# Kernel tuning notes

Measured on AMD Instinct MI355X. Metric: run time of the kernel, lower is better.

The kernel has to match this reference:

```python
import jax, jax.numpy as jnp
import numpy as np
from jax import lax

IOU_THRESHOLD = 0.5
TOP = 1000


def setup_inputs() -> dict:
    key = jax.random.key(0)
    k1, k2, k3, k4, k5 = jax.random.split(key, 5)
    B, P = 16, 20000
    # valid (x1, y1, x2, y2) boxes on an ~800x800 image
    x1 = jax.random.uniform(k1, (B, P)) * 800.0
    y1 = jax.random.uniform(k2, (B, P)) * 800.0
    w = jax.random.uniform(k3, (B, P)) * 200.0 + 1.0
    h = jax.random.uniform(k4, (B, P)) * 200.0 + 1.0
    reg = jnp.stack([x1, y1, x1 + w, y1 + h], axis=-1)  # [B, P, 4]
    cls = jax.random.normal(k5, (B, P))                  # [B, P]
    return {"reg": reg, "cls": cls}


def _pairwise_iou(boxes):
    """boxes: [B, N, 4] (x1,y1,x2,y2) -> IoU [B, N, N]."""
    a = boxes[:, :, None, :]  # [B, N, 1, 4]
    b = boxes[:, None, :, :]  # [B, 1, N, 4]
    xx1 = jnp.maximum(a[..., 0], b[..., 0])
    yy1 = jnp.maximum(a[..., 1], b[..., 1])
    xx2 = jnp.minimum(a[..., 2], b[..., 2])
    yy2 = jnp.minimum(a[..., 3], b[..., 3])
    inter = jnp.clip(xx2 - xx1, 0.0) * jnp.clip(yy2 - yy1, 0.0)
    area_a = (a[..., 2] - a[..., 0]) * (a[..., 3] - a[..., 1])
    area_b = (b[..., 2] - b[..., 0]) * (b[..., 3] - b[..., 1])
    return inter / (area_a + area_b - inter)


def reference(reg, cls):
    B = cls.shape[0]
    # sort by confidence descending, gather boxes, keep top
    order = jnp.argsort(-cls, axis=1)                      # [B, P]
    sorted_cls = jnp.take_along_axis(cls, order, axis=1)[:, :TOP]            # [B, N]
    sorted_reg = jnp.take_along_axis(reg, order[:, :, None], axis=1)[:, :TOP]  # [B, N, 4]
    N = sorted_cls.shape[1]

    iou = _pairwise_iou(sorted_reg)                        # [B, N, N]

    # sequential greedy suppression: if box i still kept, drop boxes with IoU>=thr
    def body(mask, i):
        keep_i = mask[:, i]                                # [B]
        tmp = iou[:, i, :] < IOU_THRESHOLD                 # [B, N]
        upd = (mask & tmp).at[:, i].set(True)
        new_mask = jnp.where(keep_i[:, None], upd, mask)
        return new_mask, None

    mask0 = jnp.ones((B, N), dtype=bool)
    mask, _ = lax.scan(body, mask0, jnp.arange(N))

    out_reg = jnp.where(mask[:, :, None], sorted_reg, 0.0)
    out_cls = jnp.where(mask, sorted_cls, 0.0)
    return out_reg, out_cls
```

## Files before the change

### kernel.cpp

```cpp
#include <hip/hip_runtime.h>
#include <stdint.h>

#define BATCH 16
#define NPTS  20000
#define TOPK  1000
#define NKPT  20
#define NBIN  2048
#define NCOPY 4
#define CANDCAP 2048

__device__ __forceinline__ uint32_t key_desc(float f) {
    uint32_t u = __float_as_uint(f);
    uint32_t m = (u & 0x80000000u) ? ~u : (u | 0x80000000u);
    return ~m;
}

__device__ __forceinline__ float key_undo(uint32_t k) {
    uint32_t m = ~k;
    uint32_t u = (m & 0x80000000u) ? (m & 0x7FFFFFFFu) : ~m;
    return __uint_as_float(u);
}

__device__ __forceinline__ void push64(bool pred, uint64_t val, int* cntr,
                                       uint64_t* list, int lane) {
    uint64_t mask = __ballot(pred);
    if (mask) {
        int first = __ffsll((long long)mask) - 1;
        int base = 0;
        if (lane == first) base = atomicAdd(cntr, (int)__popcll(mask));
        base = __shfl(base, first);
        if (pred) {
            int off = (int)__popcll(mask & ((1ull << lane) - 1ull));
            list[base + off] = val;
        }
    }
}

__device__ __forceinline__ void wave_select(const uint64_t* lst, int n, int r,
                                            uint64_t* out, int wave, int lane) {
    if (wave == 0) {
        uint64_t my = (lane < n) ? lst[lane] : ~0ull;
        int rank = 0;
        for (int i = 0; i < n; ++i) { uint64_t o = __shfl(my, i); if (o < my) rank++; }
        if (lane < n && rank == r) *out = my;
    }
}

__device__ uint64_t bit_search(const uint32_t* kreg, uint64_t known, uint64_t kmask,
                               int startbit, uint32_t r, int* sh_c,
                               int tid, int lane) {
    for (int bit = startbit; bit >= 0; --bit) {
        if (tid == 0) *sh_c = 0;
        __syncthreads();
        uint32_t local = 0;
        #pragma unroll
        for (int j = 0; j < NKPT; ++j) {
            int p = tid + j * 1024;
            uint64_t k64 = ((uint64_t)kreg[j] << 32) | (uint32_t)p;
            if (p < NPTS && (k64 & kmask) == known && !((k64 >> bit) & 1ull)) local++;
        }
        #pragma unroll
        for (int d = 1; d < 64; d <<= 1) local += __shfl_xor(local, d);
        if (lane == 0 && local) atomicAdd(sh_c, (int)local);
        __syncthreads();
        uint32_t c0 = (uint32_t)*sh_c;
        if (r >= c0) { known |= 1ull << bit; r -= c0; }
        kmask |= 1ull << bit;
        __syncthreads();
    }
    return known;
}

__device__ __forceinline__ void hist_scan_find(
    uint32_t (*wh)[NBIN], uint32_t* wsum, uint32_t* wpre,
    int* sh_T, int* sh_r, int* sh_binc,
    int tid, int wave, int lane, uint32_t r)
{
    uint32_t m0 = 0, m1 = 0;
    #pragma unroll
    for (int cpy = 0; cpy < NCOPY; ++cpy) { m0 += wh[cpy][2*tid]; m1 += wh[cpy][2*tid+1]; }
    uint32_t s = m0 + m1, x = s;
    #pragma unroll
    for (int d = 1; d < 64; d <<= 1) { uint32_t t = __shfl_up(x, d); if (lane >= d) x += t; }
    if (lane == 63) wsum[wave] = x;
    __syncthreads();
    if (wave == 0 && lane < 16) {
        uint32_t v = wsum[lane], y = v;
        #pragma unroll
        for (int d = 1; d < 16; d <<= 1) { uint32_t t = __shfl_up(y, d); if (lane >= d) y += t; }
        wpre[lane] = y - v;
    }
    __syncthreads();
    uint32_t e = wpre[wave] + (x - s);
    if (r >= e && r < e + s) {
        if (r < e + m0) { *sh_T = 2*tid;     *sh_r = (int)(r - e);      *sh_binc = (int)m0; }
        else            { *sh_T = 2*tid + 1; *sh_r = (int)(r - e - m0); *sh_binc = (int)m1; }
    }
}

__global__ __launch_bounds__(1024, 4) void topk_kernel(
    const float* __restrict__ reg, const float* __restrict__ cls,
    float4* __restrict__ ws_boxes, float* __restrict__ ws_cls)
{
    __shared__ uint32_t whist[NCOPY][NBIN];
    __shared__ uint32_t wsum[16], wpre[16];
    __shared__ int      sh_T, sh_r, sh_binc, sh_cnt, sh_c;
    __shared__ uint64_t sh_kthkey;
    __shared__ uint64_t cand[CANDCAP];
    __shared__ uint64_t cand2[64];
    __shared__ uint64_t sel[1024];

    const int b = blockIdx.x, tid = threadIdx.x;
    const int wave = tid >> 6, lane = tid & 63;
    const float* c = cls + (size_t)b * NPTS;

    if (tid == 0) { sh_cnt = 0; }

    #pragma unroll
    for (int i = 0; i < NCOPY * NBIN / 1024; ++i) ((uint32_t*)whist)[tid + i * 1024] = 0;
    uint32_t kreg[NKPT];
    #pragma unroll
    for (int j = 0; j < NKPT; ++j) {
        int p = tid + j * 1024;
        kreg[j] = (p < NPTS) ? key_desc(c[p]) : 0xFFFFFFFFu;
    }
    __syncthreads();

    #pragma unroll
    for (int j = 0; j < NKPT; ++j) {
        int p = tid + j * 1024;
        if (p < NPTS) atomicAdd(&whist[wave >> 2][kreg[j] >> 21], 1u);
    }
    __syncthreads();
    hist_scan_find(whist, wsum, wpre, &sh_T, &sh_r, &sh_binc, tid, wave, lane, TOPK - 1);
    __syncthreads();
    const uint32_t T1 = (uint32_t)sh_T;
    int r = sh_r;
    const int cnt1 = sh_binc;
    uint64_t known = (uint64_t)T1 << 53;

    if (cnt1 <= 64) {
        __syncthreads();
        #pragma unroll
        for (int j = 0; j < NKPT; ++j) {
            int p = tid + j * 1024;
            push64(p < NPTS && (kreg[j] >> 21) == T1,
                   ((uint64_t)kreg[j] << 32) | (uint32_t)p, &sh_cnt, cand2, lane);
        }
        __syncthreads();
        wave_select(cand2, cnt1, r, &sh_kthkey, wave, lane);
        __syncthreads();
    } else if (cnt1 <= CANDCAP) {
        __syncthreads();
        #pragma unroll
        for (int j = 0; j < NKPT; ++j) {
            int p = tid + j * 1024;
            push64(p < NPTS && (kreg[j] >> 21) == T1,
                   ((uint64_t)kreg[j] << 32) | (uint32_t)p, &sh_cnt, cand, lane);
        }
        __syncthreads();
        #pragma unroll
        for (int i = 0; i < NCOPY * NBIN / 1024; ++i) ((uint32_t*)whist)[tid + i * 1024] = 0;
        __syncthreads();
        for (int i = tid; i < cnt1; i += 1024)
            atomicAdd(&whist[wave >> 2][(uint32_t)((cand[i] >> 42) & 2047)], 1u);
        __syncthreads();
        hist_scan_find(whist, wsum, wpre, &sh_T, &sh_r, &sh_binc, tid, wave, lane, (uint32_t)r);
        __syncthreads();
        const uint32_t T2 = (uint32_t)sh_T; r = sh_r;
        const int cnt2 = sh_binc;
        known |= (uint64_t)T2 << 42;
        if (cnt2 <= 64) {
            if (tid == 0) sh_cnt = 0;
            __syncthreads();
            for (int i = tid; i < cnt1; i += 1024)
                push64(((cand[i] >> 42) & 2047) == (uint64_t)T2,
                       cand[i], &sh_cnt, cand2, lane);
            __syncthreads();
            wave_select(cand2, cnt2, r, &sh_kthkey, wave, lane);
            __syncthreads();
        } else {
            uint64_t kk = bit_search(kreg, known, 0xFFFFFC0000000000ull, 41,
                                     (uint32_t)r, &sh_c, tid, lane);
            if (tid == 0) sh_kthkey = kk;
            __syncthreads();
        }
    } else {
        uint64_t kk = bit_search(kreg, known, 0xFFE0000000000000ull, 52,
                                 (uint32_t)r, &sh_c, tid, lane);
        if (tid == 0) sh_kthkey = kk;
        __syncthreads();
    }
    const uint64_t kthkey = sh_kthkey;

    if (tid == 0) sh_cnt = 0;
    sel[tid] = ~0ull;
    __syncthreads();
    #pragma unroll
    for (int j = 0; j < NKPT; ++j) {
        int p = tid + j * 1024;
        uint64_t key = ((uint64_t)kreg[j] << 32) | (uint32_t)p;
        push64(p < NPTS && key <= kthkey, key, &sh_cnt, sel, lane);
    }
    __syncthreads();

    uint64_t e = sel[tid];
    #pragma unroll
    for (int k = 2; k <= 64; k <<= 1) {
        #pragma unroll
        for (int j = k >> 1; j >= 1; j >>= 1) {
            uint64_t o = __shfl_xor(e, j);
            uint64_t lo = (e < o) ? e : o;
            uint64_t hi = (e < o) ? o : e;
            bool dir   = (lane & k) == 0;
            bool upper = (lane & j) != 0;
            e = (upper == dir) ? hi : lo;
        }
    }
    sel[tid] = e;
    __syncthreads();
    int grank = lane;
    #pragma unroll 1
    for (int w2 = 0; w2 < 16; ++w2) {
        if (w2 == wave) continue;
        const uint64_t* bp = &sel[w2 * 64];
        int cf = 0;
        #pragma unroll
        for (int s = 32; s >= 1; s >>= 1) {
            int t2 = cf + s;
            if (bp[t2 - 1] < e) cf = t2;
        }
        if (bp[cf] < e) cf++;
        grank += cf;
    }
    if (e != ~0ull) {
        int p = (int)(e & 0xFFFFFFFFull);
        ws_boxes[b * TOPK + grank] = ((const float4*)reg)[(size_t)b * NPTS + p];
        ws_cls[b * TOPK + grank] = key_undo((uint32_t)(e >> 32));
    }
}

__global__ __launch_bounds__(256) void iou_kernel(
    const float4* __restrict__ ws_boxes, uint32_t* __restrict__ suppT)
{
    __shared__ float4 boxes[TOPK];
    __shared__ float  areas[TOPK];
    const int b   = blockIdx.y;
    const int j   = blockIdx.x;
    const int tid = threadIdx.x;
    for (int i = tid; i < TOPK; i += 256) {
        float4 v = ws_boxes[b * TOPK + i];
        boxes[i] = v;
        areas[i] = (v.z - v.x) * (v.w - v.y);
    }
    __syncthreads();

    const int lane = tid & 63;
    const int wave = tid >> 6;
    uint32_t* t = suppT + (size_t)b * 32 * 1024;

    for (int k = wave; ; k += 4) {
        const int i = j + (k << 4);
        if (i >= TOPK) break;
        float4 a = boxes[i];
        float areaA = areas[i];
        uint64_t mine = 0;
        for (int w2 = i >> 6; w2 < 16; ++w2) {
            int col = (w2 << 6) | lane;
            bool sup = false;
            if (col < TOPK) {
                float4 bb = boxes[col];
                float xx1 = fmaxf(a.x, bb.x);
                float yy1 = fmaxf(a.y, bb.y);
                float xx2 = fminf(a.z, bb.z);
                float yy2 = fminf(a.w, bb.w);
                float iw = fmaxf(xx2 - xx1, 0.0f);
                float ih = fmaxf(yy2 - yy1, 0.0f);
                float inter = iw * ih;
                float iou = inter / (areaA + areas[col] - inter);
                sup = (iou >= 0.5f);
            }
            uint64_t m = __ballot(sup);
            if (lane == w2) mine = m;
        }
        if (lane < 16) {
            t[(2 * lane + 0) * 1024 + i] = (uint32_t)(mine & 0xFFFFFFFFull);
            t[(2 * lane + 1) * 1024 + i] = (uint32_t)(mine >> 32);
        }
    }
}

__global__ __launch_bounds__(64) void sweep_kernel(
    const uint32_t* __restrict__ suppT, const float4* __restrict__ ws_boxes,
    const float* __restrict__ ws_cls, float* __restrict__ out)
{
    const int b    = blockIdx.x;
    const int lane = threadIdx.x;
    const int myw  = lane & 31;
    const uint32_t* base = suppT + (size_t)b * 32 * 1024;

    uint32_t remv = 0, keptw = 0;
    uint4 dgA[8], clA[8], dgB[8], clB[8];

#define LOADG(W, DG, CL) { \
    const uint4* dp_ = (const uint4*)(base + (W) * 1024 + (W) * 32); \
    const uint4* cp_ = (const uint4*)(base + myw * 1024 + (W) * 32); \
    _Pragma("unroll") \
    for (int k_ = 0; k_ < 8; ++k_) { DG[k_] = dp_[k_]; CL[k_] = cp_[k_]; } }

#define STEP(D, C, BBIT) { \
    uint32_t live_ = (((~cur) >> (BBIT)) & 1u) & (uint32_t)((BBIT) < nb); \
    uint32_t msk_ = (uint32_t)0 - live_; \
    kmask |= (live_ << (BBIT)); \
    cur  |= (D) & msk_; \
    acc  |= (C) & msk_; }

#define PROC(W, DG, CL) { \
    const int nb = ((W) == 31) ? (TOPK - 31 * 32) : 32; \
    uint32_t cur = __shfl(remv, (W)); \
    uint32_t kmask = 0, acc = 0; \
    _Pragma("unroll") \
    for (int k_ = 0; k_ < 8; ++k_) { \
        STEP(DG[k_].x, CL[k_].x, 4 * k_ + 0); \
        STEP(DG[k_].y, CL[k_].y, 4 * k_ + 1); \
        STEP(DG[k_].z, CL[k_].z, 4 * k_ + 2); \
        STEP(DG[k_].w, CL[k_].w, 4 * k_ + 3); \
    } \
    remv |= acc; \
    if (myw == (W)) keptw = kmask; }

    LOADG(0, dgA, clA);
    #pragma unroll 1
    for (int w2 = 0; w2 < 16; ++w2) {
        const int wE = 2 * w2, wO = 2 * w2 + 1;
        LOADG(wO, dgB, clB);
        PROC(wE, dgA, clA);
        if (wO + 1 < 32) LOADG(wO + 1, dgA, clA);
        PROC(wO, dgB, clB);
    }

    __shared__ uint32_t skept[32];
    if (lane < 32) skept[lane] = keptw;
    __syncthreads();

    const float4* bx = ws_boxes + (size_t)b * TOPK;
    const float*  bc = ws_cls + (size_t)b * TOPK;
    float4* outr = (float4*)out + (size_t)b * TOPK;
    float*  outc = out + (size_t)BATCH * TOPK * 4 + (size_t)b * TOPK;
    for (int i = lane; i < TOPK; i += 64) {
        uint32_t keep = (skept[i >> 5] >> (i & 31)) & 1u;
        float4 v = bx[i];
        float cv = bc[i];
        outr[i] = keep ? v : make_float4(0.f, 0.f, 0.f, 0.f);
        outc[i] = keep ? cv : 0.0f;
    }
#undef LOADG
#undef STEP
#undef PROC
}

extern "C" void kernel_launch(void* const* d_in, const int* in_sizes, int n_in,
                              void* d_out, int out_size, void* d_ws, size_t ws_size,
                              hipStream_t stream) {
    (void)in_sizes; (void)n_in; (void)out_size; (void)ws_size;
    const float* reg = (const float*)d_in[0];
    const float* cls = (const float*)d_in[1];
    float* out = (float*)d_out;
    char* ws = (char*)d_ws;

    float4*   ws_boxes = (float4*)ws;
    float*    ws_cls   = (float*)(ws + 256000);
    uint32_t* suppT    = (uint32_t*)(ws + 320000);

    topk_kernel<<<dim3(BATCH), dim3(1024), 0, stream>>>(reg, cls, ws_boxes, ws_cls);
    iou_kernel<<<dim3(16, BATCH), dim3(256), 0, stream>>>(ws_boxes, suppT);
    sweep_kernel<<<dim3(BATCH), dim3(64), 0, stream>>>(suppT, ws_boxes, ws_cls, out);
}
```

Baseline: 83.35 us.

## Simplify top-k threshold selection with single-pass candidate split and brute-force rank

The top-k kernel now fuses key loading with the first histogram pass. It also replaces the second-level histogram refinement with one push pass. That pass sends keys from bins below the threshold bin straight into the selection buffer and collects threshold-bin keys into a candidate list. The exact k-th key is then found by an O(n^2) rank count over the candidates, which removes several barriers and the second histogram round but costs quadratic work when the threshold bin is large. The launch-bounds occupancy hint is also dropped.

```diff
diff --git a/kernel.cpp b/kernel.cpp
--- a/kernel.cpp
+++ b/kernel.cpp
@@ -36,16 +36,6 @@
     }
 }
 
-__device__ __forceinline__ void wave_select(const uint64_t* lst, int n, int r,
-                                            uint64_t* out, int wave, int lane) {
-    if (wave == 0) {
-        uint64_t my = (lane < n) ? lst[lane] : ~0ull;
-        int rank = 0;
-        for (int i = 0; i < n; ++i) { uint64_t o = __shfl(my, i); if (o < my) rank++; }
-        if (lane < n && rank == r) *out = my;
-    }
-}
-
 __device__ uint64_t bit_search(const uint32_t* kreg, uint64_t known, uint64_t kmask,
                                int startbit, uint32_t r, int* sh_c,
                                int tid, int lane) {
@@ -98,111 +88,78 @@
     }
 }
 
-__global__ __launch_bounds__(1024, 4) void topk_kernel(
+__global__ __launch_bounds__(1024) void topk_kernel(
     const float* __restrict__ reg, const float* __restrict__ cls,
     float4* __restrict__ ws_boxes, float* __restrict__ ws_cls)
 {
     __shared__ uint32_t whist[NCOPY][NBIN];
     __shared__ uint32_t wsum[16], wpre[16];
-    __shared__ int      sh_T, sh_r, sh_binc, sh_cnt, sh_c;
+    __shared__ int      sh_T, sh_r, sh_binc, sh_cnt, sh_cnt2, sh_c;
     __shared__ uint64_t sh_kthkey;
     __shared__ uint64_t cand[CANDCAP];
-    __shared__ uint64_t cand2[64];
     __shared__ uint64_t sel[1024];
 
     const int b = blockIdx.x, tid = threadIdx.x;
     const int wave = tid >> 6, lane = tid & 63;
     const float* c = cls + (size_t)b * NPTS;
 
-    if (tid == 0) { sh_cnt = 0; }
-
+    if (tid == 0) { sh_cnt = 0; sh_cnt2 = 0; }
+    sel[tid] = ~0ull;
     #pragma unroll
     for (int i = 0; i < NCOPY * NBIN / 1024; ++i) ((uint32_t*)whist)[tid + i * 1024] = 0;
+    __syncthreads();
+
     uint32_t kreg[NKPT];
     #pragma unroll
     for (int j = 0; j < NKPT; ++j) {
         int p = tid + j * 1024;
-        kreg[j] = (p < NPTS) ? key_desc(c[p]) : 0xFFFFFFFFu;
-    }
-    __syncthreads();
-
-    #pragma unroll
-    for (int j = 0; j < NKPT; ++j) {
-        int p = tid + j * 1024;
-        if (p < NPTS) atomicAdd(&whist[wave >> 2][kreg[j] >> 21], 1u);
+        uint32_t k = (p < NPTS) ? key_desc(c[p]) : 0xFFFFFFFFu;
+        kreg[j] = k;
+        if (p < NPTS) atomicAdd(&whist[wave >> 2][k >> 21], 1u);
     }
     __syncthreads();
     hist_scan_find(whist, wsum, wpre, &sh_T, &sh_r, &sh_binc, tid, wave, lane, TOPK - 1);
     __syncthreads();
     const uint32_t T1 = (uint32_t)sh_T;
-    int r = sh_r;
-    const int cnt1 = sh_binc;
-    uint64_t known = (uint64_t)T1 << 53;
-
-    if (cnt1 <= 64) {
-        __syncthreads();
+    const int r = sh_r, cnt1 = sh_binc;
+
+    if (cnt1 <= CANDCAP) {
         #pragma unroll
         for (int j = 0; j < NKPT; ++j) {
             int p = tid + j * 1024;
-            push64(p < NPTS && (kreg[j] >> 21) == T1,
-                   ((uint64_t)kreg[j] << 32) | (uint32_t)p, &sh_cnt, cand2, lane);
-        }
-        __syncthreads();
-        wave_select(cand2, cnt1, r, &sh_kthkey, wave, lane);
-        __syncthreads();
-    } else if (cnt1 <= CANDCAP) {
-        __syncthreads();
+            uint32_t k = kreg[j];
+            uint64_t key = ((uint64_t)k << 32) | (uint32_t)p;
+            bool valid = (p < NPTS);
+            uint32_t bin = k >> 21;
+            push64(valid && bin < T1, key, &sh_cnt, sel, lane);
+            push64(valid && bin == T1, key, &sh_cnt2, cand, lane);
+        }
+        __syncthreads();
+        for (int i = tid; i < cnt1; i += 1024) {
+            uint64_t e = cand[i];
+            int rk = 0;
+            for (int q = 0; q < cnt1; ++q) rk += (cand[q] < e) ? 1 : 0;
+            if (rk == r) sh_kthkey = e;
+        }
+        __syncthreads();
+        const uint64_t kth = sh_kthkey;
+        for (int i = tid; i < cnt1; i += 1024)
+            push64(cand[i] <= kth, cand[i], &sh_cnt, sel, lane);
+        __syncthreads();
+    } else {
+        uint64_t kk = bit_search(kreg, (uint64_t)T1 << 53, 0xFFE0000000000000ull,
+                                 52, (uint32_t)r, &sh_c, tid, lane);
+        if (tid == 0) { sh_kthkey = kk; sh_cnt = 0; }
+        __syncthreads();
+        const uint64_t kth = sh_kthkey;
         #pragma unroll
         for (int j = 0; j < NKPT; ++j) {
             int p = tid + j * 1024;
-            push64(p < NPTS && (kreg[j] >> 21) == T1,
-                   ((uint64_t)kreg[j] << 32) | (uint32_t)p, &sh_cnt, cand, lane);
-        }
-        __syncthreads();
-        #pragma unroll
-        for (int i = 0; i < NCOPY * NBIN / 1024; ++i) ((uint32_t*)whist)[tid + i * 1024] = 0;
-        __syncthreads();
-        for (int i = tid; i < cnt1; i += 1024)
-            atomicAdd(&whist[wave >> 2][(uint32_t)((cand[i] >> 42) & 2047)], 1u);
-        __syncthreads();
-        hist_scan_find(whist, wsum, wpre, &sh_T, &sh_r, &sh_binc, tid, wave, lane, (uint32_t)r);
-        __syncthreads();
-        const uint32_t T2 = (uint32_t)sh_T; r = sh_r;
-        const int cnt2 = sh_binc;
-        known |= (uint64_t)T2 << 42;
-        if (cnt2 <= 64) {
-            if (tid == 0) sh_cnt = 0;
-            __syncthreads();
-            for (int i = tid; i < cnt1; i += 1024)
-                push64(((cand[i] >> 42) & 2047) == (uint64_t)T2,
-                       cand[i], &sh_cnt, cand2, lane);
-            __syncthreads();
-            wave_select(cand2, cnt2, r, &sh_kthkey, wave, lane);
-            __syncthreads();
-        } else {
-            uint64_t kk = bit_search(kreg, known, 0xFFFFFC0000000000ull, 41,
-                                     (uint32_t)r, &sh_c, tid, lane);
-            if (tid == 0) sh_kthkey = kk;
-            __syncthreads();
-        }
-    } else {
-        uint64_t kk = bit_search(kreg, known, 0xFFE0000000000000ull, 52,
-                                 (uint32_t)r, &sh_c, tid, lane);
-        if (tid == 0) sh_kthkey = kk;
-        __syncthreads();
-    }
-    const uint64_t kthkey = sh_kthkey;
-
-    if (tid == 0) sh_cnt = 0;
-    sel[tid] = ~0ull;
-    __syncthreads();
-    #pragma unroll
-    for (int j = 0; j < NKPT; ++j) {
-        int p = tid + j * 1024;
-        uint64_t key = ((uint64_t)kreg[j] << 32) | (uint32_t)p;
-        push64(p < NPTS && key <= kthkey, key, &sh_cnt, sel, lane);
-    }
-    __syncthreads();
+            uint64_t key = ((uint64_t)kreg[j] << 32) | (uint32_t)p;
+            push64(p < NPTS && key <= kth, key, &sh_cnt, sel, lane);
+        }
+        __syncthreads();
+    }
 
     uint64_t e = sel[tid];
     #pragma unroll
@@ -217,6 +174,7 @@
             e = (upper == dir) ? hi : lo;
         }
     }
+    __syncthreads();
     sel[tid] = e;
     __syncthreads();
     int grank = lane;
```

Measured after the change: 216.5 us. +159.8%, slower.
